# Kernel optimization log

Hardware: AMD Instinct MI355X
Metric: run time of the kernel (lower is better)

The kernel has to match this reference:

```python
import jax, jax.numpy as jnp
import numpy as np

NUM_EMBEDDINGS = 1024
EMBEDDING_DIM = 64
COMMITMENT_COST = 0.25


def setup_inputs() -> dict:
    key = jax.random.key(0)
    k1, k2 = jax.random.split(key)
    z = jax.random.normal(k1, (32, 64, 64, 64), dtype=jnp.float32)  # [B, C=D, H, W]
    # module initializes embedding ~ Uniform(-1/K, 1/K)
    embedding = jax.random.uniform(
        k2, (NUM_EMBEDDINGS, EMBEDDING_DIM), dtype=jnp.float32,
        minval=-1.0 / NUM_EMBEDDINGS, maxval=1.0 / NUM_EMBEDDINGS)
    return {"z": z, "embedding": embedding}


def reference(z, embedding):
    B, C, H, W = z.shape
    K = embedding.shape[0]
    zp = jnp.transpose(z, (0, 2, 3, 1))          # b h w c
    z_flat = zp.reshape(-1, C)                   # [N, D]

    # L2 distances: ||z||^2 + ||e||^2 - 2 z e^T   -> [N, K]
    distances = (jnp.sum(z_flat * z_flat, axis=1, keepdims=True)
                 + jnp.sum(embedding * embedding, axis=1)
                 - 2.0 * jnp.matmul(z_flat, embedding.T))
    encoding_indices = jnp.argmin(distances, axis=1)          # [N] int

    # one-hot matmul lookup == direct gather (same math)
    quantized = embedding[encoding_indices].reshape(zp.shape)  # b h w c

    e_latent_loss = jnp.mean((jax.lax.stop_gradient(quantized) - zp) ** 2)
    q_latent_loss = jnp.mean((quantized - jax.lax.stop_gradient(zp)) ** 2)
    loss = q_latent_loss + COMMITMENT_COST * e_latent_loss

    # straight-through estimator
    quantized_st = zp + jax.lax.stop_gradient(quantized - zp)
    quantized_out = jnp.transpose(quantized_st, (0, 3, 1, 2))  # b c h w

    # perplexity from average code usage
    N = z_flat.shape[0]
    counts = jnp.zeros((K,), dtype=jnp.float32).at[encoding_indices].add(1.0)
    avg_probs = counts / N
    perplexity = jnp.exp(-jnp.sum(avg_probs * jnp.log(avg_probs + 1e-10)))

    return quantized_out, loss, perplexity, encoding_indices
```

## Files before the change

kernel.cpp:

```cpp
#include <hip/hip_runtime.h>
#include <math.h>


#define NROWS 131072
#define KCODES 1024
#define DDIM 64
#define CAP 16

typedef __attribute__((ext_vector_type(8))) short short8v;
typedef __attribute__((ext_vector_type(4))) float f32x4;

__device__ __forceinline__ float nofuse(float x) {
    asm("" : "+v"(x));
    return x;
}

template <typename F>
__device__ __forceinline__ float pairwise64_sq(F load) {
    float r[8];
#pragma unroll
    for (int j = 0; j < 8; j++) {
        float v = load(j);
        r[j] = nofuse(v * v);
    }
#pragma unroll
    for (int i = 8; i < 64; i += 8) {
#pragma unroll
        for (int j = 0; j < 8; j++) {
            float v = load(i + j);
            r[j] = r[j] + nofuse(v * v);
        }
    }
    return ((r[0] + r[1]) + (r[2] + r[3])) + ((r[4] + r[5]) + (r[6] + r[7]));
}

__device__ __forceinline__ unsigned short bf16_rne(float x) {
    unsigned u = __float_as_uint(x);
    u += 0x7FFFu + ((u >> 16) & 1u);
    return (unsigned short)(u >> 16);
}
__device__ __forceinline__ float bf16_tof(unsigned short h) {
    return __uint_as_float((unsigned)h << 16);
}

__global__ __launch_bounds__(256) void kE(const float* __restrict__ emb,
                                          float* __restrict__ ee,
                                          unsigned short* __restrict__ eh_p) {
    int k = blockIdx.x * 256 + threadIdx.x;
    if (k >= KCODES) return;
    const float* er = emb + (size_t)k * DDIM;
    ee[k] = pairwise64_sq([&](int i) { return er[i]; });
#pragma unroll
    for (int i = 0; i < DDIM; i++) eh_p[(size_t)k * DDIM + i] = bf16_rne(er[i]);
}

#define MFMA_BF16(acc, a, b) \
    acc = __builtin_amdgcn_mfma_f32_16x16x32_bf16(a, b, acc, 0, 0, 0)

#define DOT_TILE(ti, B0, B1, ACT)                                       \
    {                                                                   \
        const int codeL = code0 + (ti) * 16 + (l & 15);                 \
        const float eev = ee_s[codeL];                                  \
        _Pragma("unroll") for (int rt = 0; rt < 4; rt++) {              \
            f32x4 acc = {0.f, 0.f, 0.f, 0.f};                           \
            MFMA_BF16(acc, ah[rt][0], B0);                              \
            MFMA_BF16(acc, ah[rt][1], B1);                              \
            MFMA_BF16(acc, al[rt][0], B0);                              \
            MFMA_BF16(acc, al[rt][1], B1);                              \
            _Pragma("unroll") for (int r = 0; r < 4; r++) {             \
                float sv = fmaf(-2.0f, acc[r], eev);                    \
                ACT(rt, r, sv, codeL);                                  \
            }                                                           \
        }                                                               \
    }

#define ACT_MIN(rt, r, sv, code) rm[rt][r] = fminf(rm[rt][r], sv);
#define ACT_COLLECT(rt, r, sv, code)                                    \
    if (sv <= thr[rt][r]) {                                             \
        int row_ = rt * 16 + ((l >> 4) << 2) + r;                       \
        int pos_ = atomicAdd(&cnt_s[row_], 1);                          \
        if (pos_ < CAP) cand_s[row_][pos_] = (unsigned short)(code);    \
    }

__global__ __launch_bounds__(256) void kA2(const float* __restrict__ z,
                                           const float* __restrict__ emb,
                                           const float* __restrict__ ee,
                                           const unsigned short* __restrict__ eh_p,
                                           int* __restrict__ counts,
                                           float* __restrict__ out_idx,
                                           float* __restrict__ out_q,
                                           double* __restrict__ loss_sum) {
    __shared__ float zt[64][65];
    __shared__ float ee_s[KCODES];
    __shared__ float zz_s[64];
    __shared__ float wq_s[64];
    __shared__ float rmw_s[4][64];
    __shared__ int cnt_s[64];
    __shared__ unsigned short cand_s[64][CAP];
    __shared__ int idx_s[64];
    __shared__ double wred[4];

    const int tid = threadIdx.x;
    const int blk = blockIdx.x;
    const int n0 = blk * 64;
    const int b = blk >> 6;
    const int h = blk & 63;

    const float* zb = z + (size_t)b * 262144 + (size_t)h * 64;
    for (int i = tid; i < 64 * 64; i += 256) {
        int d = i >> 6, w = i & 63;
        zt[w][d] = zb[(size_t)d * 4096 + w];
    }
    for (int i = tid; i < KCODES; i += 256) ee_s[i] = ee[i];
    __syncthreads();

    if (tid < 64) {
        const int w = tid;
        zz_s[w] = pairwise64_sq([&](int i) { return zt[w][i]; });
        float s = 0.0f;
#pragma unroll
        for (int i = 0; i < 64; i++) s += fabsf(zt[w][i]);
        wq_s[w] = fmaf(1e-5f, s, 1e-4f);
        cnt_s[w] = 0;
    }
    __syncthreads();

    const int wv = tid >> 6;
    const int l = tid & 63;
    const int kg = (l >> 4) * 8;
    const int code0 = wv * 256;

    short8v ah[4][2], al[4][2];
#pragma unroll
    for (int rt = 0; rt < 4; rt++) {
        const int arow = rt * 16 + (l & 15);
#pragma unroll
        for (int kt = 0; kt < 2; kt++) {
#pragma unroll
            for (int i = 0; i < 8; i++) {
                float x = zt[arow][kt * 32 + kg + i];
                unsigned short hh = bf16_rne(x);
                ah[rt][kt][i] = (short)hh;
                al[rt][kt][i] = (short)bf16_rne(x - bf16_tof(hh));
            }
        }
    }

    const unsigned short* ebase = eh_p + (size_t)code0 * 64;

    float rm[4][4];
#pragma unroll
    for (int rt = 0; rt < 4; rt++)
#pragma unroll
        for (int r = 0; r < 4; r++) rm[rt][r] = INFINITY;

    {
        short8v b0A, b1A, b0B, b1B;
        const unsigned short* p0 = ebase + (size_t)(l & 15) * 64 + kg;
        b0A = *(const short8v*)p0;
        b1A = *(const short8v*)(p0 + 32);
#pragma unroll 4
        for (int ti = 0; ti < 16; ti++) {
            if (ti < 15) {
                const unsigned short* p =
                    ebase + (size_t)((ti + 1) * 16 + (l & 15)) * 64 + kg;
                b0B = *(const short8v*)p;
                b1B = *(const short8v*)(p + 32);
            }
            DOT_TILE(ti, b0A, b1A, ACT_MIN)
            if (ti < 15) { b0A = b0B; b1A = b1B; }
        }
    }
#pragma unroll
    for (int rt = 0; rt < 4; rt++)
#pragma unroll
        for (int r = 0; r < 4; r++) {
            float v = rm[rt][r];
            v = fminf(v, __shfl_xor(v, 1, 64));
            v = fminf(v, __shfl_xor(v, 2, 64));
            v = fminf(v, __shfl_xor(v, 4, 64));
            v = fminf(v, __shfl_xor(v, 8, 64));
            rm[rt][r] = v;
        }
    if ((l & 15) == 0) {
#pragma unroll
        for (int rt = 0; rt < 4; rt++)
#pragma unroll
            for (int r = 0; r < 4; r++)
                rmw_s[wv][rt * 16 + ((l >> 4) << 2) + r] = rm[rt][r];
    }
    __syncthreads();

    float thr[4][4];
#pragma unroll
    for (int rt = 0; rt < 4; rt++)
#pragma unroll
        for (int r = 0; r < 4; r++) {
            const int row = rt * 16 + ((l >> 4) << 2) + r;
            float m01 = fminf(rmw_s[0][row], rmw_s[1][row]);
            float m23 = fminf(rmw_s[2][row], rmw_s[3][row]);
            thr[rt][r] = fminf(m01, m23) + wq_s[row];
        }

    {
        short8v b0A, b1A, b0B, b1B;
        const unsigned short* p0 = ebase + (size_t)(l & 15) * 64 + kg;
        b0A = *(const short8v*)p0;
        b1A = *(const short8v*)(p0 + 32);
#pragma unroll 4
        for (int ti = 0; ti < 16; ti++) {
            if (ti < 15) {
                const unsigned short* p =
                    ebase + (size_t)((ti + 1) * 16 + (l & 15)) * 64 + kg;
                b0B = *(const short8v*)p;
                b1B = *(const short8v*)(p + 32);
            }
            DOT_TILE(ti, b0A, b1A, ACT_COLLECT)
            if (ti < 15) { b0A = b0B; b1A = b1B; }
        }
    }
    __syncthreads();

    if (tid < 64) {
        const int w = tid;
        const float zzv = zz_s[w];
        float bv = INFINITY;
        int bi = 0;
        const int nc = cnt_s[w];
        if (nc > CAP) {
            for (int k = 0; k < KCODES; k++) {
                const float* er = emb + (size_t)k * 64;
                float dot = 0.0f;
#pragma unroll
                for (int d = 0; d < 64; d++)
                    dot = __builtin_fmaf(zt[w][d], er[d], dot);
                float tt = zzv + ee_s[k];
                float dv = tt - 2.0f * dot;
                if (dv < bv || (dv == bv && k < bi)) { bv = dv; bi = k; }
            }
        } else {
            for (int j = 0; j < nc; j++) {
                const int k = cand_s[w][j];
                const float* er = emb + (size_t)k * 64;
                float dot = 0.0f;
#pragma unroll
                for (int d = 0; d < 64; d++)
                    dot = __builtin_fmaf(zt[w][d], er[d], dot);
                float tt = zzv + ee_s[k];
                float dv = tt - 2.0f * dot;
                if (dv < bv || (dv == bv && k < bi)) { bv = dv; bi = k; }
            }
        }
        idx_s[w] = bi;
        out_idx[n0 + w] = (float)bi;
        atomicAdd(&counts[bi], 1);
    }
    __syncthreads();

    float* qb = out_q + (size_t)b * 262144 + (size_t)h * 64;
    double dsum = 0.0;
    for (int i = tid; i < 4096; i += 256) {
        int c = i >> 6, w = i & 63;
        float q = emb[(size_t)idx_s[w] * 64 + c];
        float zv = zt[w][c];
        qb[(size_t)c * 4096 + w] = q;
        float df = q - zv;
        float s = df * df;
        dsum += (double)s;
    }
    for (int off = 32; off > 0; off >>= 1) dsum += __shfl_down(dsum, off, 64);
    if ((tid & 63) == 0) wred[tid >> 6] = dsum;
    __syncthreads();
    if (tid == 0) {
        double tot = (wred[0] + wred[1]) + (wred[2] + wred[3]);
        atomicAdd(loss_sum, tot);
    }
}

__global__ __launch_bounds__(1024) void kC(const int* __restrict__ counts,
                                           const double* __restrict__ loss_sum,
                                           float* __restrict__ out_loss,
                                           float* __restrict__ out_perp) {
    __shared__ float wr[16];
    const int tid = threadIdx.x;
    float p = (float)counts[tid] * (1.0f / 131072.0f);
    float v = p + 1e-10f;
    float term = p * logf(v);
    float s = term;
    for (int off = 32; off > 0; off >>= 1) s += __shfl_down(s, off, 64);
    if ((tid & 63) == 0) wr[tid >> 6] = s;
    __syncthreads();
    if (tid == 0) {
        float tot = 0.0f;
#pragma unroll
        for (int j = 0; j < 16; j++) tot += wr[j];
        out_perp[0] = expf(-tot);
        double L = *loss_sum / 8388608.0;
        float Lf = (float)L;
        out_loss[0] = Lf + 0.25f * Lf;
    }
}

extern "C" void kernel_launch(void* const* d_in, const int* in_sizes, int n_in,
                              void* d_out, int out_size, void* d_ws, size_t ws_size,
                              hipStream_t stream) {
    const float* z = (const float*)d_in[0];
    const float* emb = (const float*)d_in[1];
    float* out = (float*)d_out;
    float* out_q = out;
    float* out_loss = out + 8388608;
    float* out_perp = out + 8388609;
    float* out_idx = out + 8388610;

    char* ws = (char*)d_ws;
    double* loss_sum = (double*)ws;
    int* counts = (int*)(ws + 64);
    float* ee = (float*)(ws + 64 + 4096);
    unsigned short* eh_p = (unsigned short*)(ws + 64 + 8192);

    hipMemsetAsync(d_ws, 0, 64 + 4096, stream);
    kE<<<4, 256, 0, stream>>>(emb, ee, eh_p);
    kA2<<<2048, 256, 0, stream>>>(z, emb, ee, eh_p, counts, out_idx, out_q,
                                  loss_sum);
    kC<<<1, 1024, 0, stream>>>(counts, loss_sum, out_loss, out_perp);
}
```

Before: 158.4 us.

## Drop bf16 split-precision MFMA term, double rows per block, deepen B prefetch

Removes the low-order bf16 correction MFMAs, so the distance screen uses single bf16 products, and widens the candidate margin to offset the lower precision. Each block now handles 128 rows instead of 64, halving the grid and reusing each codebook B fragment across twice as many rows. The codebook loads use a 3-deep register prefetch ring, and the exact fp32 rescoring reads the codebook as float4. The risks are more candidates overflowing CAP and falling back to the full 1024-code scan, plus higher register and LDS use that lowers occupancy.

```diff
diff --git a/kernel.cpp b/kernel.cpp
--- a/kernel.cpp
+++ b/kernel.cpp
@@ -38,9 +38,6 @@
     unsigned u = __float_as_uint(x);
     u += 0x7FFFu + ((u >> 16) & 1u);
     return (unsigned short)(u >> 16);
-}
-__device__ __forceinline__ float bf16_tof(unsigned short h) {
-    return __uint_as_float((unsigned)h << 16);
 }
 
 __global__ __launch_bounds__(256) void kE(const float* __restrict__ emb,
@@ -61,12 +58,10 @@
     {                                                                   \
         const int codeL = code0 + (ti) * 16 + (l & 15);                 \
         const float eev = ee_s[codeL];                                  \
-        _Pragma("unroll") for (int rt = 0; rt < 4; rt++) {              \
+        _Pragma("unroll") for (int rt = 0; rt < 8; rt++) {              \
             f32x4 acc = {0.f, 0.f, 0.f, 0.f};                           \
             MFMA_BF16(acc, ah[rt][0], B0);                              \
             MFMA_BF16(acc, ah[rt][1], B1);                              \
-            MFMA_BF16(acc, al[rt][0], B0);                              \
-            MFMA_BF16(acc, al[rt][1], B1);                              \
             _Pragma("unroll") for (int r = 0; r < 4; r++) {             \
                 float sv = fmaf(-2.0f, acc[r], eev);                    \
                 ACT(rt, r, sv, codeL);                                  \
@@ -76,10 +71,18 @@
 
 #define ACT_MIN(rt, r, sv, code) rm[rt][r] = fminf(rm[rt][r], sv);
 #define ACT_COLLECT(rt, r, sv, code)                                    \
-    if (sv <= thr[rt][r]) {                                             \
+    if (sv <= thr_r[rt][r]) {                                           \
         int row_ = rt * 16 + ((l >> 4) << 2) + r;                       \
         int pos_ = atomicAdd(&cnt_s[row_], 1);                          \
         if (pos_ < CAP) cand_s[row_][pos_] = (unsigned short)(code);    \
+    }
+
+#define PRE_B(ti)                                                       \
+    {                                                                   \
+        const unsigned short* p_ =                                      \
+            ebase + (size_t)((ti) * 16 + (l & 15)) * 64 + kg;           \
+        pb0[(ti) % 3] = *(const short8v*)p_;                            \
+        pb1[(ti) % 3] = *(const short8v*)(p_ + 32);                     \
     }
 
 __global__ __launch_bounds__(256) void kA2(const float* __restrict__ z,
@@ -90,37 +93,38 @@
                                            float* __restrict__ out_idx,
                                            float* __restrict__ out_q,
                                            double* __restrict__ loss_sum) {
-    __shared__ float zt[64][65];
+    __shared__ float zt[128][65];
     __shared__ float ee_s[KCODES];
-    __shared__ float zz_s[64];
-    __shared__ float wq_s[64];
-    __shared__ float rmw_s[4][64];
-    __shared__ int cnt_s[64];
-    __shared__ unsigned short cand_s[64][CAP];
-    __shared__ int idx_s[64];
+    __shared__ float zz_s[128];
+    __shared__ float wq_s[128];
+    __shared__ float rmw_s[4][128];
+    __shared__ float thr_s[128];
+    __shared__ int cnt_s[128];
+    __shared__ unsigned short cand_s[128][CAP];
+    __shared__ int idx_s[128];
     __shared__ double wred[4];
 
     const int tid = threadIdx.x;
     const int blk = blockIdx.x;
-    const int n0 = blk * 64;
-    const int b = blk >> 6;
-    const int h = blk & 63;
-
-    const float* zb = z + (size_t)b * 262144 + (size_t)h * 64;
-    for (int i = tid; i < 64 * 64; i += 256) {
-        int d = i >> 6, w = i & 63;
-        zt[w][d] = zb[(size_t)d * 4096 + w];
+    const int n0 = blk * 128;
+    const int b = blk >> 5;
+    const int h0 = (blk & 31) * 2;
+
+    const float* zb = z + (size_t)b * 262144 + (size_t)h0 * 64;
+    for (int i = tid; i < 128 * 64; i += 256) {
+        int d = i >> 7, j = i & 127;
+        zt[j][d] = zb[(size_t)d * 4096 + j];
     }
     for (int i = tid; i < KCODES; i += 256) ee_s[i] = ee[i];
     __syncthreads();
 
-    if (tid < 64) {
+    if (tid < 128) {
         const int w = tid;
         zz_s[w] = pairwise64_sq([&](int i) { return zt[w][i]; });
         float s = 0.0f;
 #pragma unroll
         for (int i = 0; i < 64; i++) s += fabsf(zt[w][i]);
-        wq_s[w] = fmaf(1e-5f, s, 1e-4f);
+        wq_s[w] = fmaf(2e-5f, s, 1e-4f);
         cnt_s[w] = 0;
     }
     __syncthreads();
@@ -130,49 +134,37 @@
     const int kg = (l >> 4) * 8;
     const int code0 = wv * 256;
 
-    short8v ah[4][2], al[4][2];
-#pragma unroll
-    for (int rt = 0; rt < 4; rt++) {
+    short8v ah[8][2];
+#pragma unroll
+    for (int rt = 0; rt < 8; rt++) {
         const int arow = rt * 16 + (l & 15);
 #pragma unroll
         for (int kt = 0; kt < 2; kt++) {
 #pragma unroll
-            for (int i = 0; i < 8; i++) {
-                float x = zt[arow][kt * 32 + kg + i];
-                unsigned short hh = bf16_rne(x);
-                ah[rt][kt][i] = (short)hh;
-                al[rt][kt][i] = (short)bf16_rne(x - bf16_tof(hh));
-            }
+            for (int i = 0; i < 8; i++)
+                ah[rt][kt][i] = (short)bf16_rne(zt[arow][kt * 32 + kg + i]);
         }
     }
 
     const unsigned short* ebase = eh_p + (size_t)code0 * 64;
 
-    float rm[4][4];
-#pragma unroll
-    for (int rt = 0; rt < 4; rt++)
+    float rm[8][4];
+#pragma unroll
+    for (int rt = 0; rt < 8; rt++)
 #pragma unroll
         for (int r = 0; r < 4; r++) rm[rt][r] = INFINITY;
-
     {
-        short8v b0A, b1A, b0B, b1B;
-        const unsigned short* p0 = ebase + (size_t)(l & 15) * 64 + kg;
-        b0A = *(const short8v*)p0;
-        b1A = *(const short8v*)(p0 + 32);
-#pragma unroll 4
+        short8v pb0[3], pb1[3];
+        PRE_B(0)
+        PRE_B(1)
+#pragma unroll
         for (int ti = 0; ti < 16; ti++) {
-            if (ti < 15) {
-                const unsigned short* p =
-                    ebase + (size_t)((ti + 1) * 16 + (l & 15)) * 64 + kg;
-                b0B = *(const short8v*)p;
-                b1B = *(const short8v*)(p + 32);
-            }
-            DOT_TILE(ti, b0A, b1A, ACT_MIN)
-            if (ti < 15) { b0A = b0B; b1A = b1B; }
-        }
-    }
-#pragma unroll
-    for (int rt = 0; rt < 4; rt++)
+            if (ti + 2 < 16) PRE_B(ti + 2)
+            DOT_TILE(ti, pb0[ti % 3], pb1[ti % 3], ACT_MIN)
+        }
+    }
+#pragma unroll
+    for (int rt = 0; rt < 8; rt++)
 #pragma unroll
         for (int r = 0; r < 4; r++) {
             float v = rm[rt][r];
@@ -184,44 +176,39 @@
         }
     if ((l & 15) == 0) {
 #pragma unroll
-        for (int rt = 0; rt < 4; rt++)
+        for (int rt = 0; rt < 8; rt++)
 #pragma unroll
             for (int r = 0; r < 4; r++)
                 rmw_s[wv][rt * 16 + ((l >> 4) << 2) + r] = rm[rt][r];
     }
     __syncthreads();
-
-    float thr[4][4];
-#pragma unroll
-    for (int rt = 0; rt < 4; rt++)
-#pragma unroll
-        for (int r = 0; r < 4; r++) {
-            const int row = rt * 16 + ((l >> 4) << 2) + r;
-            float m01 = fminf(rmw_s[0][row], rmw_s[1][row]);
-            float m23 = fminf(rmw_s[2][row], rmw_s[3][row]);
-            thr[rt][r] = fminf(m01, m23) + wq_s[row];
-        }
+    if (tid < 128) {
+        float m01 = fminf(rmw_s[0][tid], rmw_s[1][tid]);
+        float m23 = fminf(rmw_s[2][tid], rmw_s[3][tid]);
+        thr_s[tid] = fminf(m01, m23) + wq_s[tid];
+    }
+    __syncthreads();
+
+    float thr_r[8][4];
+#pragma unroll
+    for (int rt = 0; rt < 8; rt++)
+#pragma unroll
+        for (int r = 0; r < 4; r++)
+            thr_r[rt][r] = thr_s[rt * 16 + ((l >> 4) << 2) + r];
 
     {
-        short8v b0A, b1A, b0B, b1B;
-        const unsigned short* p0 = ebase + (size_t)(l & 15) * 64 + kg;
-        b0A = *(const short8v*)p0;
-        b1A = *(const short8v*)(p0 + 32);
-#pragma unroll 4
+        short8v pb0[3], pb1[3];
+        PRE_B(0)
+        PRE_B(1)
+#pragma unroll
         for (int ti = 0; ti < 16; ti++) {
-            if (ti < 15) {
-                const unsigned short* p =
-                    ebase + (size_t)((ti + 1) * 16 + (l & 15)) * 64 + kg;
-                b0B = *(const short8v*)p;
-                b1B = *(const short8v*)(p + 32);
-            }
-            DOT_TILE(ti, b0A, b1A, ACT_COLLECT)
-            if (ti < 15) { b0A = b0B; b1A = b1B; }
-        }
-    }
-    __syncthreads();
-
-    if (tid < 64) {
+            if (ti + 2 < 16) PRE_B(ti + 2)
+            DOT_TILE(ti, pb0[ti % 3], pb1[ti % 3], ACT_COLLECT)
+        }
+    }
+    __syncthreads();
+
+    if (tid < 128) {
         const int w = tid;
         const float zzv = zz_s[w];
         float bv = INFINITY;
@@ -229,11 +216,16 @@
         const int nc = cnt_s[w];
         if (nc > CAP) {
             for (int k = 0; k < KCODES; k++) {
-                const float* er = emb + (size_t)k * 64;
+                const float4* er = (const float4*)(emb + (size_t)k * 64);
                 float dot = 0.0f;
 #pragma unroll
-                for (int d = 0; d < 64; d++)
-                    dot = __builtin_fmaf(zt[w][d], er[d], dot);
+                for (int q = 0; q < 16; q++) {
+                    float4 e4 = er[q];
+                    dot = __builtin_fmaf(zt[w][4 * q + 0], e4.x, dot);
+                    dot = __builtin_fmaf(zt[w][4 * q + 1], e4.y, dot);
+                    dot = __builtin_fmaf(zt[w][4 * q + 2], e4.z, dot);
+                    dot = __builtin_fmaf(zt[w][4 * q + 3], e4.w, dot);
+                }
                 float tt = zzv + ee_s[k];
                 float dv = tt - 2.0f * dot;
                 if (dv < bv || (dv == bv && k < bi)) { bv = dv; bi = k; }
@@ -241,11 +233,16 @@
         } else {
             for (int j = 0; j < nc; j++) {
                 const int k = cand_s[w][j];
-                const float* er = emb + (size_t)k * 64;
+                const float4* er = (const float4*)(emb + (size_t)k * 64);
                 float dot = 0.0f;
 #pragma unroll
-                for (int d = 0; d < 64; d++)
-                    dot = __builtin_fmaf(zt[w][d], er[d], dot);
+                for (int q = 0; q < 16; q++) {
+                    float4 e4 = er[q];
+                    dot = __builtin_fmaf(zt[w][4 * q + 0], e4.x, dot);
+                    dot = __builtin_fmaf(zt[w][4 * q + 1], e4.y, dot);
+                    dot = __builtin_fmaf(zt[w][4 * q + 2], e4.z, dot);
+                    dot = __builtin_fmaf(zt[w][4 * q + 3], e4.w, dot);
+                }
                 float tt = zzv + ee_s[k];
                 float dv = tt - 2.0f * dot;
                 if (dv < bv || (dv == bv && k < bi)) { bv = dv; bi = k; }
@@ -257,13 +254,13 @@
     }
     __syncthreads();
 
-    float* qb = out_q + (size_t)b * 262144 + (size_t)h * 64;
+    float* qb = out_q + (size_t)b * 262144 + (size_t)h0 * 64;
     double dsum = 0.0;
-    for (int i = tid; i < 4096; i += 256) {
-        int c = i >> 6, w = i & 63;
-        float q = emb[(size_t)idx_s[w] * 64 + c];
-        float zv = zt[w][c];
-        qb[(size_t)c * 4096 + w] = q;
+    for (int i = tid; i < 128 * 64; i += 256) {
+        int c = i >> 7, j = i & 127;
+        float q = emb[(size_t)idx_s[j] * 64 + c];
+        float zv = zt[j][c];
+        qb[(size_t)c * 4096 + j] = q;
         float df = q - zv;
         float s = df * df;
         dsum += (double)s;
@@ -320,7 +317,7 @@
 
     hipMemsetAsync(d_ws, 0, 64 + 4096, stream);
     kE<<<4, 256, 0, stream>>>(emb, ee, eh_p);
-    kA2<<<2048, 256, 0, stream>>>(z, emb, ee, eh_p, counts, out_idx, out_q,
+    kA2<<<1024, 256, 0, stream>>>(z, emb, ee, eh_p, counts, out_idx, out_q,
                                   loss_sum);
     kC<<<1, 1024, 0, stream>>>(counts, loss_sum, out_loss, out_perp);
 }
```

Measured after the change: 183.2 us. 15.7% more time.
